# Performance work log

Measured on AMD Instinct MI355X. Metric: run time of the kernel, lower is better.

The kernel has to match this reference:

```python
import jax, jax.numpy as jnp
import numpy as np

B, N, C = 16, 1024, 1024
H = 16            # num_attention_heads
D = C // H        # attention_head_size = 64

def setup_inputs() -> dict:
    key = jax.random.key(0)
    k1, k2, k3 = jax.random.split(key, 3)
    scale = 1.0 / np.sqrt(C)
    return {
        "hidden_states": jax.random.normal(k1, (B, N, C), dtype=jnp.float32),
        "qkv_w": jax.random.normal(k2, (C, 3 * C), dtype=jnp.float32) * scale,
        "qkv_b": jnp.zeros((3 * C,), dtype=jnp.float32),
        "proj_w": jax.random.normal(k3, (C, C), dtype=jnp.float32) * scale,
        "proj_b": jnp.zeros((C,), dtype=jnp.float32),
    }

def reference(hidden_states, qkv_w, qkv_b, proj_w, proj_b):
    # fused QKV projection: [B, N, 3C]
    qkv = hidden_states @ qkv_w + qkv_b
    # reshape to [3, B, H, N, D]
    qkv = qkv.reshape(B, N, 3, H, D).transpose(2, 0, 3, 1, 4)
    q, k, v = qkv[0], qkv[1], qkv[2]
    # attention scores [B, H, N, N]
    scores = jnp.einsum("bhnd,bhmd->bhnm", q, k) / jnp.sqrt(jnp.float32(D))
    probs = jax.nn.softmax(scores, axis=-1)  # dropout_p=0 -> identity
    ctx = jnp.einsum("bhnm,bhmd->bhnd", probs, v)
    ctx = ctx.transpose(0, 2, 1, 3).reshape(B, N, C)
    # output projection
    return ctx @ proj_w + proj_b
```

## Files before the change

kernel.cpp:

```cpp
#include <hip/hip_runtime.h>


#define BB 16
#define NN 1024
#define CC 1024
#define HH 16
#define DD 64
#define BN (BB * NN)
#define HEADELEMS (256 * 1024 * 64)

typedef float  f4     __attribute__((ext_vector_type(4)));
typedef __bf16 bf16x8 __attribute__((ext_vector_type(8)));
typedef __bf16 bf16x4 __attribute__((ext_vector_type(4)));
typedef short  s8v    __attribute__((ext_vector_type(8)));
typedef short  s4v    __attribute__((ext_vector_type(4)));
typedef short  s2v    __attribute__((ext_vector_type(2)));

__device__ __forceinline__ short f2bf(float x) {
  union { float f; unsigned u; } a; a.f = x;
  unsigned r = a.u + 0x7fffu + ((a.u >> 16) & 1u);
  return (short)(r >> 16);
}

__device__ __forceinline__ void gl_lds16(const void* g, void* l) {
  __builtin_amdgcn_global_load_lds((__attribute__((address_space(1))) void*)g,
                                   (__attribute__((address_space(3))) void*)l,
                                   16, 0, 0);
}

__device__ __forceinline__ f4 mfma16(bf16x8 a, bf16x8 b, f4 c) {
  return __builtin_amdgcn_mfma_f32_16x16x32_bf16(a, b, c, 0, 0, 0);
}

__global__ void cast_bf16(const float* __restrict__ x, short* __restrict__ y) {
  int i = (blockIdx.x * 256 + threadIdx.x) * 4;
  float4 v = *(const float4*)&x[i];
  s4v o;
  o[0] = f2bf(v.x); o[1] = f2bf(v.y); o[2] = f2bf(v.z); o[3] = f2bf(v.w);
  *(s4v*)&y[i] = o;
}

__global__ void transpose_cast(const float* __restrict__ W, short* __restrict__ Wt,
                               int K, int Nw) {
  __shared__ float tile[32][33];
  int bx = blockIdx.x, by = blockIdx.y;
  int t = threadIdx.x;
  int tc = t & 31, tr = t >> 5;
#pragma unroll
  for (int i = 0; i < 4; ++i) {
    int r = tr + i * 8;
    tile[r][tc] = W[(size_t)(by * 32 + r) * Nw + bx * 32 + tc];
  }
  __syncthreads();
#pragma unroll
  for (int i = 0; i < 4; ++i) {
    int r = tr + i * 8;
    Wt[(size_t)(bx * 32 + r) * K + by * 32 + tc] = f2bf(tile[tc][r]);
  }
}

template <int EPI>
__global__ __launch_bounds__(256, 2)
void gemm_bt(const short* __restrict__ A, const short* __restrict__ Bt,
             const float* __restrict__ bias, float* __restrict__ Cf,
             short* __restrict__ Cq, int M, int N, int K) {
  __shared__ short la[128 * 64];
  __shared__ short lb[128 * 64];
  const int t = threadIdx.x, lane = t & 63, w = t >> 6;
  const int row0 = blockIdx.y * 128, col0 = blockIdx.x * 128;
  const int wm = (w & 1) * 64, wn = (w >> 1) * 64;
  const int q = lane >> 4, ln = lane & 15;
  const int sr8 = lane >> 3;
  const int sc8 = (lane & 7) ^ sr8;
  f4 acc[4][4] = {};

  for (int kb = 0; kb < K; kb += 64) {
    __syncthreads();
#pragma unroll
    for (int rblk = 0; rblk < 4; ++rblk) {
      int rbase = (w * 4 + rblk) * 8;
      const short* ga = A + (size_t)(row0 + rbase + sr8) * K + kb + sc8 * 8;
      const short* gb = Bt + (size_t)(col0 + rbase + sr8) * K + kb + sc8 * 8;
      gl_lds16(ga, &la[rbase * 64]);
      gl_lds16(gb, &lb[rbase * 64]);
    }
    __syncthreads();
#pragma unroll
    for (int ks2 = 0; ks2 < 2; ++ks2) {
      const int c8 = ks2 * 4 + q;
      const int sw = (c8 ^ (ln & 7)) * 8;
      bf16x8 af[4], bfr[4];
#pragma unroll
      for (int i = 0; i < 4; ++i) {
        af[i]  = *(const bf16x8*)&la[(wm + i * 16 + ln) * 64 + sw];
        bfr[i] = *(const bf16x8*)&lb[(wn + i * 16 + ln) * 64 + sw];
      }
#pragma unroll
      for (int i = 0; i < 4; ++i)
#pragma unroll
        for (int j = 0; j < 4; ++j)
          acc[i][j] = mfma16(af[i], bfr[j], acc[i][j]);
    }
  }

#pragma unroll
  for (int i = 0; i < 4; ++i) {
    int rbase = row0 + wm + i * 16 + q * 4;
#pragma unroll
    for (int j = 0; j < 4; ++j) {
      int col = col0 + wn + j * 16 + ln;
      float bv = bias[col];
      if (EPI == 0) {
#pragma unroll
        for (int r2 = 0; r2 < 4; ++r2)
          Cf[(size_t)(rbase + r2) * N + col] = acc[i][j][r2] + bv;
      } else {
        int which = col >> 10, c = col & 1023;
        int h = c >> 6, d = c & 63;
        float scale = (which == 0) ? 0.1803368801f : 1.0f;
#pragma unroll
        for (int r2 = 0; r2 < 4; ++r2) {
          int row = rbase + r2;
          int bh = (row >> 10) * HH + h;
          size_t idx = ((size_t)bh * NN + (row & 1023)) * DD + d;
          Cq[(size_t)which * HEADELEMS + idx] = f2bf((acc[i][j][r2] + bv) * scale);
        }
      }
    }
  }
}

__global__ __launch_bounds__(512, 4)
void attn(const short* __restrict__ Qg, const short* __restrict__ Kg,
          const short* __restrict__ Vg, short* __restrict__ ctx) {
  __shared__ short sQP[128][72];
  __shared__ short sK[64][72];
  __shared__ short sV[64][72];
  const int t = threadIdx.x, lane = t & 63, w = t >> 6;
  const int bh = blockIdx.x, qb = blockIdx.y;
  const short* Qh = Qg + (size_t)bh * (NN * DD) + qb * 128 * DD;
  const short* Kh = Kg + (size_t)bh * (NN * DD);
  const short* Vh = Vg + (size_t)bh * (NN * DD);

  for (int i = t; i < 128 * 8; i += 512) {
    int r = i >> 3, c8 = i & 7;
    *(s8v*)&sQP[r][c8 * 8] = *(const s8v*)&Qh[r * DD + c8 * 8];
  }
  __syncthreads();

  const int q = lane >> 4, ln = lane & 15;
  const int wq = w * 16;
  bf16x8 qf[2];
  qf[0] = *(const bf16x8*)&sQP[wq + ln][q * 8];
  qf[1] = *(const bf16x8*)&sQP[wq + ln][32 + q * 8];

  f4 o[4] = {};
  float lsum = 0.f;

  for (int kt = 0; kt < 16; ++kt) {
    __syncthreads();
    if (w < 4) {
      int c8 = t >> 5, pr = t & 31;
      s8v v0 = *(const s8v*)&Vh[(kt * 64 + 2 * pr) * DD + c8 * 8];
      s8v v1 = *(const s8v*)&Vh[(kt * 64 + 2 * pr + 1) * DD + c8 * 8];
#pragma unroll
      for (int j = 0; j < 8; ++j) {
        s2v tmp; tmp[0] = v0[j]; tmp[1] = v1[j];
        *(s2v*)&sV[c8 * 8 + j][2 * pr] = tmp;
      }
    } else {
      int t2 = t - 256;
#pragma unroll
      for (int i2 = 0; i2 < 2; ++i2) {
        int i = t2 + i2 * 256;
        int r = i >> 3, c8 = i & 7;
        *(s8v*)&sK[r][c8 * 8] = *(const s8v*)&Kh[(kt * 64 + r) * DD + c8 * 8];
      }
    }
    __syncthreads();

    f4 s[4] = {};
#pragma unroll
    for (int ks = 0; ks < 2; ++ks) {
#pragma unroll
      for (int ki = 0; ki < 4; ++ki) {
        bf16x8 kf = *(const bf16x8*)&sK[ki * 16 + ln][ks * 32 + q * 8];
        s[ki] = mfma16(kf, qf[ks], s[ki]);
      }
    }

#pragma unroll
    for (int ki = 0; ki < 4; ++ki) {
      float p0 = exp2f(s[ki][0]), p1 = exp2f(s[ki][1]);
      float p2 = exp2f(s[ki][2]), p3 = exp2f(s[ki][3]);
      lsum += (p0 + p1) + (p2 + p3);
      bf16x4 pk;
      pk[0] = (__bf16)p0; pk[1] = (__bf16)p1;
      pk[2] = (__bf16)p2; pk[3] = (__bf16)p3;
      *(bf16x4*)&sQP[wq + ln][ki * 16 + q * 4] = pk;
    }

#pragma unroll
    for (int ks = 0; ks < 2; ++ks) {
      bf16x8 pf = *(const bf16x8*)&sQP[wq + ln][ks * 32 + q * 8];
#pragma unroll
      for (int j = 0; j < 4; ++j) {
        bf16x8 vf = *(const bf16x8*)&sV[j * 16 + ln][ks * 32 + q * 8];
        o[j] = mfma16(pf, vf, o[j]);
      }
    }
  }

  float lfull = lsum;
  lfull += __shfl_xor(lfull, 16);
  lfull += __shfl_xor(lfull, 32);

#pragma unroll
  for (int r = 0; r < 4; ++r) {
    float lr = __shfl(lfull, q * 4 + r);
    float inv = 1.0f / lr;
    int token_row = qb * 128 + wq + q * 4 + r;
    size_t base = ((size_t)(bh >> 4) * NN + token_row) * CC + (bh & 15) * DD;
#pragma unroll
    for (int j = 0; j < 4; ++j)
      ctx[base + j * 16 + ln] = f2bf(o[j][r] * inv);
  }
}

extern "C" void kernel_launch(void* const* d_in, const int* in_sizes, int n_in,
                              void* d_out, int out_size, void* d_ws, size_t ws_size,
                              hipStream_t stream) {
  const float* hs     = (const float*)d_in[0];
  const float* qkv_w  = (const float*)d_in[1];
  const float* qkv_b  = (const float*)d_in[2];
  const float* proj_w = (const float*)d_in[3];
  const float* proj_b = (const float*)d_in[4];

  short* ws = (short*)d_ws;
  if (ws_size < 176160768ull) return;
  short* Xbf = ws;
  short* Wq  = ws + 16777216;
  short* Wp  = ws + 19922944;
  short* Qm  = ws + 20971520;
  short* Km  = ws + 37748736;
  short* Vm  = ws + 54525952;
  short* Ctx = ws + 71303168;

  cast_bf16<<<16384, 256, 0, stream>>>(hs, Xbf);
  transpose_cast<<<dim3(96, 32), 256, 0, stream>>>(qkv_w, Wq, 1024, 3072);
  transpose_cast<<<dim3(32, 32), 256, 0, stream>>>(proj_w, Wp, 1024, 1024);

  gemm_bt<1><<<dim3(24, 128), 256, 0, stream>>>(Xbf, Wq, qkv_b, nullptr, Qm,
                                                BN, 3 * CC, CC);
  attn<<<dim3(256, 8), 512, 0, stream>>>(Qm, Km, Vm, Ctx);
  gemm_bt<0><<<dim3(8, 128), 256, 0, stream>>>(Ctx, Wp, proj_b, (float*)d_out, nullptr,
                                               BN, CC, CC);
}
```

Before: 410.5 us.

## Double-buffer attention K/V tiles with async LDS loads and pre-transposed V

```diff
diff --git a/kernel.cpp b/kernel.cpp
--- a/kernel.cpp
+++ b/kernel.cpp
@@ -56,6 +56,30 @@
   for (int i = 0; i < 4; ++i) {
     int r = tr + i * 8;
     Wt[(size_t)(bx * 32 + r) * K + by * 32 + tc] = f2bf(tile[tc][r]);
+  }
+}
+
+__global__ void transpose_v(const short* __restrict__ Vm, short* __restrict__ Vt) {
+  __shared__ short tile[64][68];
+  int bh = blockIdx.x, n0 = blockIdx.y * 64;
+  const short* src = Vm + (size_t)bh * (NN * DD) + (size_t)n0 * DD;
+  short* dst = Vt + (size_t)bh * (NN * DD) + n0;
+  int t = threadIdx.x;
+#pragma unroll
+  for (int i2 = 0; i2 < 2; ++i2) {
+    int i = t + i2 * 256;
+    int r = i >> 3, c = i & 7;
+    *(s8v*)&tile[r][c * 8] = *(const s8v*)&src[(size_t)r * DD + c * 8];
+  }
+  __syncthreads();
+#pragma unroll
+  for (int i2 = 0; i2 < 2; ++i2) {
+    int i = t + i2 * 256;
+    int d = i >> 3, c = i & 7;
+    s8v v;
+#pragma unroll
+    for (int j = 0; j < 8; ++j) v[j] = tile[c * 8 + j][d];
+    *(s8v*)&dst[(size_t)d * NN + c * 8] = v;
   }
 }
 
@@ -132,62 +156,60 @@
 
 __global__ __launch_bounds__(512, 4)
 void attn(const short* __restrict__ Qg, const short* __restrict__ Kg,
-          const short* __restrict__ Vg, short* __restrict__ ctx) {
-  __shared__ short sQP[128][72];
-  __shared__ short sK[64][72];
-  __shared__ short sV[64][72];
+          const short* __restrict__ Vtg, short* __restrict__ ctx) {
+  __shared__ short sQP[128 * 64];
+  __shared__ short sK[2][64 * 64];
+  __shared__ short sV[2][64 * 64];
   const int t = threadIdx.x, lane = t & 63, w = t >> 6;
   const int bh = blockIdx.x, qb = blockIdx.y;
   const short* Qh = Qg + (size_t)bh * (NN * DD) + qb * 128 * DD;
   const short* Kh = Kg + (size_t)bh * (NN * DD);
-  const short* Vh = Vg + (size_t)bh * (NN * DD);
-
-  for (int i = t; i < 128 * 8; i += 512) {
-    int r = i >> 3, c8 = i & 7;
-    *(s8v*)&sQP[r][c8 * 8] = *(const s8v*)&Qh[r * DD + c8 * 8];
-  }
+  const short* Vh = Vtg + (size_t)bh * (NN * DD);
+
+  {
+    int r0 = t >> 3, c0 = t & 7;
+    gl_lds16(Qh + r0 * DD + ((c0 ^ (r0 & 7)) * 8), &sQP[t * 8]);
+    int i1 = t + 512;
+    int r1 = i1 >> 3, c1 = i1 & 7;
+    gl_lds16(Qh + r1 * DD + ((c1 ^ (r1 & 7)) * 8), &sQP[i1 * 8]);
+  }
+  const int sr = t >> 3, sc = t & 7;
+  const int ssc = ((sc ^ (sr & 7)) * 8);
+  gl_lds16(Kh + sr * DD + ssc, &sK[0][t * 8]);
+  gl_lds16(Vh + (size_t)sr * NN + ssc, &sV[0][t * 8]);
+
   __syncthreads();
 
   const int q = lane >> 4, ln = lane & 15;
   const int wq = w * 16;
+  const int sw = ln & 7;
+
   bf16x8 qf[2];
-  qf[0] = *(const bf16x8*)&sQP[wq + ln][q * 8];
-  qf[1] = *(const bf16x8*)&sQP[wq + ln][32 + q * 8];
+  qf[0] = *(const bf16x8*)&sQP[(wq + ln) * 64 + ((0 + q) ^ sw) * 8];
+  qf[1] = *(const bf16x8*)&sQP[(wq + ln) * 64 + ((4 + q) ^ sw) * 8];
 
   f4 o[4] = {};
   float lsum = 0.f;
 
   for (int kt = 0; kt < 16; ++kt) {
-    __syncthreads();
-    if (w < 4) {
-      int c8 = t >> 5, pr = t & 31;
-      s8v v0 = *(const s8v*)&Vh[(kt * 64 + 2 * pr) * DD + c8 * 8];
-      s8v v1 = *(const s8v*)&Vh[(kt * 64 + 2 * pr + 1) * DD + c8 * 8];
-#pragma unroll
-      for (int j = 0; j < 8; ++j) {
-        s2v tmp; tmp[0] = v0[j]; tmp[1] = v1[j];
-        *(s2v*)&sV[c8 * 8 + j][2 * pr] = tmp;
-      }
-    } else {
-      int t2 = t - 256;
-#pragma unroll
-      for (int i2 = 0; i2 < 2; ++i2) {
-        int i = t2 + i2 * 256;
-        int r = i >> 3, c8 = i & 7;
-        *(s8v*)&sK[r][c8 * 8] = *(const s8v*)&Kh[(kt * 64 + r) * DD + c8 * 8];
-      }
-    }
-    __syncthreads();
+    const int cur = kt & 1;
+    if (kt < 15) {
+      const int nb = cur ^ 1;
+      gl_lds16(Kh + (kt + 1) * 64 * DD + sr * DD + ssc, &sK[nb][t * 8]);
+      gl_lds16(Vh + (size_t)sr * NN + (kt + 1) * 64 + ssc, &sV[nb][t * 8]);
+    }
 
     f4 s[4] = {};
+    __builtin_amdgcn_s_setprio(1);
 #pragma unroll
     for (int ks = 0; ks < 2; ++ks) {
 #pragma unroll
       for (int ki = 0; ki < 4; ++ki) {
-        bf16x8 kf = *(const bf16x8*)&sK[ki * 16 + ln][ks * 32 + q * 8];
+        bf16x8 kf = *(const bf16x8*)&sK[cur][(ki * 16 + ln) * 64 + (((ks * 4 + q) ^ sw) * 8)];
         s[ki] = mfma16(kf, qf[ks], s[ki]);
       }
     }
+    __builtin_amdgcn_s_setprio(0);
 
 #pragma unroll
     for (int ki = 0; ki < 4; ++ki) {
@@ -197,18 +219,22 @@
       bf16x4 pk;
       pk[0] = (__bf16)p0; pk[1] = (__bf16)p1;
       pk[2] = (__bf16)p2; pk[3] = (__bf16)p3;
-      *(bf16x4*)&sQP[wq + ln][ki * 16 + q * 4] = pk;
-    }
-
+      *(bf16x4*)&sQP[(wq + ln) * 64 + (((2 * ki + (q >> 1)) ^ sw) * 8) + (q & 1) * 4] = pk;
+    }
+
+    __builtin_amdgcn_s_setprio(1);
 #pragma unroll
     for (int ks = 0; ks < 2; ++ks) {
-      bf16x8 pf = *(const bf16x8*)&sQP[wq + ln][ks * 32 + q * 8];
+      bf16x8 pf = *(const bf16x8*)&sQP[(wq + ln) * 64 + (((ks * 4 + q) ^ sw) * 8)];
 #pragma unroll
       for (int j = 0; j < 4; ++j) {
-        bf16x8 vf = *(const bf16x8*)&sV[j * 16 + ln][ks * 32 + q * 8];
+        bf16x8 vf = *(const bf16x8*)&sV[cur][(j * 16 + ln) * 64 + (((ks * 4 + q) ^ sw) * 8)];
         o[j] = mfma16(pf, vf, o[j]);
       }
     }
+    __builtin_amdgcn_s_setprio(0);
+
+    __syncthreads();
   }
 
   float lfull = lsum;
@@ -245,6 +271,7 @@
   short* Km  = ws + 37748736;
   short* Vm  = ws + 54525952;
   short* Ctx = ws + 71303168;
+  short* Vt  = Xbf;
 
   cast_bf16<<<16384, 256, 0, stream>>>(hs, Xbf);
   transpose_cast<<<dim3(96, 32), 256, 0, stream>>>(qkv_w, Wq, 1024, 3072);
@@ -252,7 +279,8 @@
 
   gemm_bt<1><<<dim3(24, 128), 256, 0, stream>>>(Xbf, Wq, qkv_b, nullptr, Qm,
                                                 BN, 3 * CC, CC);
-  attn<<<dim3(256, 8), 512, 0, stream>>>(Qm, Km, Vm, Ctx);
+  transpose_v<<<dim3(256, 16), 256, 0, stream>>>(Vm, Vt);
+  attn<<<dim3(256, 8), 512, 0, stream>>>(Qm, Km, Vt, Ctx);
   gemm_bt<0><<<dim3(8, 128), 256, 0, stream>>>(Ctx, Wp, proj_b, (float*)d_out, nullptr,
                                                BN, CC, CC);
 }
```

Result: slower. 420.8 us (+2.5%).
